# Kernel tuning notes

Measured on AMD Instinct MI355X. Metric: run time of the kernel, lower is better.

Reference implementation:

```python
import jax, jax.numpy as jnp
import numpy as np

B, C, H, W, E = 2, 4, 56, 56, 768
NH = 12
HD = E // NH
WS = 14
MLP_DIM = 3072
EPS = 1e-5


def layernorm(x, w, b):
    mu = jnp.mean(x, axis=-1, keepdims=True)
    var = jnp.mean((x - mu) ** 2, axis=-1, keepdims=True)
    return (x - mu) * jax.lax.rsqrt(var + EPS) * w + b


def setup_inputs() -> dict:
    key = jax.random.key(0)
    ks = jax.random.split(key, 12)
    s = 0.02
    return {
        "x": jax.random.normal(ks[0], (B, C, H, W, E), dtype=jnp.float32),
        "norm1_w": jnp.ones((E,), jnp.float32),
        "norm1_b": jnp.zeros((E,), jnp.float32),
        "qkv_w": jax.random.normal(ks[1], (E, 3 * E), jnp.float32) * s,
        "qkv_b": jnp.zeros((3 * E,), jnp.float32),
        "proj_w": jax.random.normal(ks[2], (E, E), jnp.float32) * s,
        "proj_b": jnp.zeros((E,), jnp.float32),
        "rel_pos_h": jax.random.normal(ks[3], (2 * WS - 1, HD), jnp.float32) * s,
        "rel_pos_w": jax.random.normal(ks[4], (2 * WS - 1, HD), jnp.float32) * s,
        "norm2_w": jnp.ones((E,), jnp.float32),
        "norm2_b": jnp.zeros((E,), jnp.float32),
        "mlp_w1": jax.random.normal(ks[5], (E, MLP_DIM), jnp.float32) * s,
        "mlp_b1": jnp.zeros((MLP_DIM,), jnp.float32),
        "mlp_w2": jax.random.normal(ks[6], (MLP_DIM, E), jnp.float32) * s,
        "mlp_b2": jnp.zeros((E,), jnp.float32),
    }


def reference(x, norm1_w, norm1_b, qkv_w, qkv_b, proj_w, proj_b,
              rel_pos_h, rel_pos_w, norm2_w, norm2_b,
              mlp_w1, mlp_b1, mlp_w2, mlp_b2):
    b, c, h, w, e = x.shape
    scale = HD ** -0.5
    shortcut = x

    y = x.reshape(b * c, h, w, e)
    y = layernorm(y, norm1_w, norm1_b)

    pad_h = (-h) % WS
    pad_w = (-w) % WS
    if pad_h or pad_w:
        y = jnp.pad(y, ((0, 0), (0, pad_h), (0, pad_w), (0, 0)))
    hp, wp = h + pad_h, w + pad_w
    y = y.reshape(b * c, hp // WS, WS, wp // WS, WS, e)
    y = y.transpose(0, 1, 3, 2, 4, 5).reshape(-1, WS, WS, e)  # [Bw, WS, WS, E]
    bw = y.shape[0]
    n = WS * WS

    # qkv projection
    qkv = y.reshape(bw, n, e) @ qkv_w + qkv_b
    qkv = qkv.reshape(bw, n, 3, NH, HD).transpose(2, 0, 3, 1, 4).reshape(3, bw * NH, n, HD)
    q, k, v = qkv[0], qkv[1], qkv[2]

    attn = (q * scale) @ jnp.swapaxes(k, -2, -1)  # [bw*NH, n, n]

    # decomposed relative position bias (q_size == k_size == WS, no interpolation)
    idx = jnp.arange(WS)[:, None] - jnp.arange(WS)[None, :] + (WS - 1)  # [WS, WS]
    Rh = rel_pos_h[idx]  # [WS, WS, HD]
    Rw = rel_pos_w[idx]
    r_q = q.reshape(-1, WS, WS, HD)
    rel_h = jnp.einsum('bhwc,hkc->bhwk', r_q, Rh)
    rel_w = jnp.einsum('bhwc,wkc->bhwk', r_q, Rw)
    attn = (attn.reshape(-1, WS, WS, WS, WS)
            + rel_h[..., :, None]
            + rel_w[:, :, :, None, :]).reshape(-1, n, n)

    attn = jax.nn.softmax(attn, axis=-1)
    out = attn @ v  # [bw*NH, n, HD]
    out = out.reshape(bw, NH, WS, WS, HD).transpose(0, 2, 3, 1, 4).reshape(bw, WS, WS, e)
    out = out @ proj_w + proj_b

    # window unpartition
    out = out.reshape(b * c, hp // WS, wp // WS, WS, WS, e)
    out = out.transpose(0, 1, 3, 2, 4, 5).reshape(b * c, hp, wp, e)
    out = out[:, :h, :w, :].reshape(b, c, h, w, e)

    x1 = shortcut + out
    z = layernorm(x1, norm2_w, norm2_b)
    z = jax.nn.gelu(z @ mlp_w1 + mlp_b1, approximate=False)
    z = z @ mlp_w2 + mlp_b2
    return x1 + z
```

## Files before the change

kernel.cpp:

```cpp
#include <hip/hip_runtime.h>
#include <math.h>

typedef unsigned short u16;
typedef __bf16 bf16x8 __attribute__((ext_vector_type(8)));
typedef float   f32x4 __attribute__((ext_vector_type(4)));
typedef u16     u16x4 __attribute__((ext_vector_type(4)));

#define TOK 25088
#define EMB 768
#define NWH 1536
#define NTOKW 196
#define PROW 224
#define PPAD 232
#define GROUP_M 4

#define OFF_VT 38535168ull
#define OFF_W0 127565824ull
#define OFF_W1 131104768ull
#define OFF_W2 132284416ull
#define OFF_W3 137003008ull
#define OFF_H  38535168ull

__device__ __forceinline__ u16 f2bf(float f) {
  __bf16 h = (__bf16)f;
  return __builtin_bit_cast(u16, h);
}

__device__ __forceinline__ float bf2f(u16 u) {
  return __builtin_bit_cast(float, (unsigned)u << 16);
}

__device__ __forceinline__ void cp16(void* lds, const void* gsrc) {
  __builtin_amdgcn_global_load_lds((const __attribute__((address_space(1))) void*)gsrc,
                                   (__attribute__((address_space(3))) void*)lds,
                                   16, 0, 0);
}

__device__ __forceinline__ f32x4 mfma16(bf16x8 a, bf16x8 b, f32x4 c) {
  return __builtin_amdgcn_mfma_f32_16x16x32_bf16(a, b, c, 0, 0, 0);
}

__global__ __launch_bounds__(256)
void transpose_w(const float* __restrict__ src, u16* __restrict__ dst, int R, int C) {
  __shared__ float tile[32][33];
  const int tx = threadIdx.x & 31;
  const int ty = threadIdx.x >> 5;
  const int c0 = blockIdx.x * 32;
  const int r0 = blockIdx.y * 32;
  #pragma unroll
  for (int i = ty; i < 32; i += 8)
    tile[i][tx] = src[(size_t)(r0 + i) * C + c0 + tx];
  __syncthreads();
  #pragma unroll
  for (int i = ty; i < 32; i += 8)
    dst[(size_t)(c0 + i) * R + r0 + tx] = f2bf(tile[tx][i]);
}

template<bool WIN>
__global__ __launch_bounds__(256)
void ln_kernel(const float* __restrict__ x, const float* __restrict__ g,
               const float* __restrict__ b, u16* __restrict__ y) {
  const int wave = threadIdx.x >> 6;
  const int lane = threadIdx.x & 63;
  const int row = blockIdx.x * 4 + wave;
  const float* xr = x + (size_t)row * EMB;
  float4 v[3];
  float s = 0.f, ss = 0.f;
  #pragma unroll
  for (int j = 0; j < 3; j++) {
    v[j] = *(const float4*)&xr[lane * 4 + j * 256];
    s  += v[j].x + v[j].y + v[j].z + v[j].w;
    ss += v[j].x*v[j].x + v[j].y*v[j].y + v[j].z*v[j].z + v[j].w*v[j].w;
  }
  #pragma unroll
  for (int off = 1; off < 64; off <<= 1) {
    s  += __shfl_xor(s, off);
    ss += __shfl_xor(ss, off);
  }
  const float mu = s * (1.0f / 768.0f);
  const float var = ss * (1.0f / 768.0f) - mu * mu;
  const float rs = rsqrtf(var + 1e-5f);
  size_t drow;
  if (WIN) {
    const int bc = row / 3136;
    const int rem = row - bc * 3136;
    const int h = rem / 56;
    const int w = rem - h * 56;
    const int window = bc * 16 + (h / 14) * 4 + (w / 14);
    const int token = (h % 14) * 14 + (w % 14);
    drow = (size_t)window * NTOKW + token;
  } else {
    drow = (size_t)row;
  }
  u16* yr = y + drow * EMB;
  #pragma unroll
  for (int j = 0; j < 3; j++) {
    const int e = lane * 4 + j * 256;
    const float4 gv = *(const float4*)&g[e];
    const float4 bv = *(const float4*)&b[e];
    u16x4 o;
    o[0] = f2bf((v[j].x - mu) * rs * gv.x + bv.x);
    o[1] = f2bf((v[j].y - mu) * rs * gv.y + bv.y);
    o[2] = f2bf((v[j].z - mu) * rs * gv.z + bv.z);
    o[3] = f2bf((v[j].w - mu) * rs * gv.w + bv.w);
    *(u16x4*)&yr[e] = o;
  }
}

#define EPI_QKV  0
#define EPI_PROJ 1
#define EPI_MLP1 2
#define EPI_MLP2 3

template<int EPI>
__global__ __launch_bounds__(512, 2)
void gemm256(const u16* __restrict__ A, const u16* __restrict__ Bt,
             int K, int moff, int nbm, int nbn,
             const float* __restrict__ bias,
             const float* __restrict__ aux,
             u16* __restrict__ o0, u16* __restrict__ o1, u16* __restrict__ o2,
             float* of) {
  __shared__ __align__(16) u16 lds[2][2][256 * 64];
  const int t = threadIdx.x;
  const int wave = t >> 6;
  const int lane = t & 63;
  const int quad = lane >> 4;
  const int l16 = lane & 15;
  const int wm = wave >> 2;
  const int wn = wave & 3;

  const int in_group = GROUP_M * nbn;
  const int gid = blockIdx.x / in_group;
  const int rem0 = blockIdx.x - gid * in_group;
  const int gm = min(GROUP_M, nbm - gid * GROUP_M);
  const int bm = gid * GROUP_M + rem0 % gm;
  const int bn = rem0 / gm;
  const int m0 = bm * 256;
  const int n0 = bn * 256;

  const int sr0 = t >> 3;
  const int sc0 = ((t ^ (t >> 3)) & 7) * 8;
  const int c1_ = t + 512;
  const int sr1 = c1_ >> 3;
  const int sc1 = ((c1_ ^ (c1_ >> 3)) & 7) * 8;
  const u16* Ag0 = A + (size_t)(m0 + sr0) * K + sc0;
  const u16* Ag1 = A + (size_t)(m0 + sr1) * K + sc1;
  const u16* Bg0 = Bt + (size_t)(n0 + sr0) * K + sc0;
  const u16* Bg1 = Bt + (size_t)(n0 + sr1) * K + sc1;
  const size_t hstep = (size_t)128 * K;

  const int cK0 = ((quad    ) ^ (l16 & 7)) * 8;
  const int cK1 = ((4 + quad) ^ (l16 & 7)) * 8;

  f32x4 acc[8][4];
  const f32x4 zero4 = {0.f, 0.f, 0.f, 0.f};
  #pragma unroll
  for (int i = 0; i < 8; i++)
    #pragma unroll
    for (int j = 0; j < 4; j++) acc[i][j] = zero4;
  bf16x8 bfr[4][2];

#define STG(bb, mat, half, G0, G1, kk) do {                                          \
    cp16(&lds[bb][mat][(half) * 8192 + wave * 512],        (G0) + (half) * hstep + (kk)); \
    cp16(&lds[bb][mat][(half) * 8192 + 4096 + wave * 512], (G1) + (half) * hstep + (kk)); \
  } while (0)

#define LOADB(bb) do {                                                               \
    _Pragma("unroll")                                                                \
    for (int nf = 0; nf < 4; nf++) {                                                 \
      bfr[nf][0] = *(const bf16x8*)&lds[bb][1][(wn * 64 + nf * 16 + l16) * 64 + cK0];\
      bfr[nf][1] = *(const bf16x8*)&lds[bb][1][(wn * 64 + nf * 16 + l16) * 64 + cK1];\
    }                                                                                \
  } while (0)

#define PHASE(bb, slab, PRE, POST) do {                                              \
    const int ar_ = (wm * 128 + (slab) * 32 + l16) * 64;                             \
    bf16x8 a00 = *(const bf16x8*)&lds[bb][0][ar_ + cK0];                             \
    bf16x8 a01 = *(const bf16x8*)&lds[bb][0][ar_ + cK1];                             \
    bf16x8 a10 = *(const bf16x8*)&lds[bb][0][ar_ + 1024 + cK0];                      \
    bf16x8 a11 = *(const bf16x8*)&lds[bb][0][ar_ + 1024 + cK1];                      \
    PRE;                                                                             \
    __builtin_amdgcn_s_barrier();                                                    \
    asm volatile("s_waitcnt lgkmcnt(0)" ::: "memory");                               \
    __builtin_amdgcn_sched_barrier(0);                                               \
    __builtin_amdgcn_s_setprio(1);                                                   \
    _Pragma("unroll")                                                                \
    for (int nf = 0; nf < 4; nf++) {                                                 \
      acc[(slab) * 2    ][nf] = mfma16(a00, bfr[nf][0], acc[(slab) * 2    ][nf]);    \
      acc[(slab) * 2    ][nf] = mfma16(a01, bfr[nf][1], acc[(slab) * 2    ][nf]);    \
      acc[(slab) * 2 + 1][nf] = mfma16(a10, bfr[nf][0], acc[(slab) * 2 + 1][nf]);    \
      acc[(slab) * 2 + 1][nf] = mfma16(a11, bfr[nf][1], acc[(slab) * 2 + 1][nf]);    \
    }                                                                                \
    __builtin_amdgcn_s_setprio(0);                                                   \
    POST;                                                                            \
    __builtin_amdgcn_s_barrier();                                                    \
  } while (0)

  STG(0, 1, 0, Bg0, Bg1, 0);  STG(0, 1, 1, Bg0, Bg1, 0);
  STG(0, 0, 0, Ag0, Ag1, 0);  STG(0, 0, 1, Ag0, Ag1, 0);
  STG(1, 1, 0, Bg0, Bg1, 64); STG(1, 1, 1, Bg0, Bg1, 64);
  asm volatile("s_waitcnt vmcnt(4)" ::: "memory");
  __builtin_amdgcn_s_barrier();

  const int T = K >> 7;
  for (int it = 0; it < T; ++it) {
    const bool nlast = (it < T - 1);
    const int kA1 = (2 * it + 1) << 6;
    const int kT2 = (2 * it + 2) << 6;
    const int kT3 = (2 * it + 3) << 6;

    LOADB(0);
    PHASE(0, 0, STG(1, 0, 0, Ag0, Ag1, kA1), );
    PHASE(0, 1, STG(1, 0, 1, Ag0, Ag1, kA1), );
    PHASE(0, 2, if (nlast) STG(0, 1, 0, Bg0, Bg1, kT2), );
    PHASE(0, 3, if (nlast) STG(0, 1, 1, Bg0, Bg1, kT2),
          if (nlast) { asm volatile("s_waitcnt vmcnt(4)" ::: "memory"); }
          else       { asm volatile("s_waitcnt vmcnt(0)" ::: "memory"); }
          __builtin_amdgcn_sched_barrier(0); );
    LOADB(1);
    PHASE(1, 0, if (nlast) STG(0, 0, 0, Ag0, Ag1, kT2), );
    PHASE(1, 1, if (nlast) STG(0, 0, 1, Ag0, Ag1, kT2), );
    PHASE(1, 2, if (nlast) STG(1, 1, 0, Bg0, Bg1, kT3), );
    PHASE(1, 3, if (nlast) STG(1, 1, 1, Bg0, Bg1, kT3),
          asm volatile("s_waitcnt vmcnt(4)" ::: "memory");
          __builtin_amdgcn_sched_barrier(0); );
  }
#undef STG
#undef LOADB
#undef PHASE

  #pragma unroll
  for (int mf = 0; mf < 8; mf++) {
    const int mb = m0 + wm * 128 + mf * 16 + quad * 4;
    #pragma unroll
    for (int nf = 0; nf < 4; nf++) {
      const int n = n0 + wn * 64 + nf * 16 + l16;
      const float bn_ = bias[n];
      if (EPI == EPI_QKV) {
        const int j3 = n / 768;
        const int rem = n - j3 * 768;
        const int head = rem >> 6;
        const int d = rem & 63;
        if (j3 == 2) {
          const int window = mb / 196;
          const int token = mb - window * 196;
          const int wh = window * 12 + head;
          u16x4 pv;
          #pragma unroll
          for (int r = 0; r < 4; r++) pv[r] = f2bf(acc[mf][nf][r] + bn_);
          *(u16x4*)&o2[((size_t)wh * 64 + d) * PROW + token] = pv;
        } else {
          u16* dst = (j3 == 0) ? o0 : o1;
          #pragma unroll
          for (int r = 0; r < 4; r++) {
            const int m = mb + r;
            const int window = m / 196;
            const int token = m - window * 196;
            const int wh = window * 12 + head;
            dst[((size_t)wh * NTOKW + token) * 64 + d] = f2bf(acc[mf][nf][r] + bn_);
          }
        }
      } else if (EPI == EPI_PROJ) {
        #pragma unroll
        for (int r = 0; r < 4; r++) {
          const int m = mb + r;
          const int window = m / 196;
          const int token = m - window * 196;
          const int bc = window >> 4;
          const int wi = window & 15;
          const int th = token / 14;
          const int tw = token - th * 14;
          const int h = (wi >> 2) * 14 + th;
          const int w = (wi & 3) * 14 + tw;
          const size_t flat = (((size_t)bc * 56 + h) * 56 + w) * 768 + n;
          of[flat] = acc[mf][nf][r] + bn_ + aux[flat];
        }
      } else if (EPI == EPI_MLP1) {
        #pragma unroll
        for (int r = 0; r < 4; r++) {
          const int m = mb + r;
          float v = acc[mf][nf][r] + bn_;
          v = 0.5f * v * (1.0f + erff(v * 0.70710678118654752f));
          o0[(size_t)m * 3072 + n] = f2bf(v);
        }
      } else {
        #pragma unroll
        for (int r = 0; r < 4; r++) {
          const int m = mb + r + moff;
          const size_t idx = (size_t)m * 768 + n;
          of[idx] = acc[mf][nf][r] + bn_ + aux[idx];
        }
      }
    }
  }
}

__global__ __launch_bounds__(256, 2)
void attn_fused(const u16* __restrict__ q, const u16* __restrict__ k,
                const u16* __restrict__ vT,
                const float* __restrict__ rph, const float* __restrict__ rpw,
                u16* __restrict__ out) {
  __shared__ __align__(16) u16 lsK[208 * 64];
  __shared__ __align__(16) u16 relh[16 * 224];
  __shared__ __align__(16) u16 relw[16 * 224];
  __shared__ __align__(16) u16 lsP[4][16 * PPAD];
  const int t = threadIdx.x;
  const int wave = t >> 6;
  const int lane = t & 63;
  const int quad = lane >> 4;
  const int l16 = lane & 15;
  const int wh = blockIdx.x;
  const u16* qg = q + (size_t)wh * (NTOKW * 64);
  const u16* kg = k + (size_t)wh * (NTOKW * 64);
  const u16* vg = vT + (size_t)wh * 64 * PROW;
  const int window = wh / 12;
  const int head = wh - window * 12;

  #pragma unroll
  for (int i = 0; i < 6; i++) {
    const int chunk = i * 256 + t;
    const int goff = ((chunk & ~7) | ((chunk ^ (chunk >> 3)) & 7)) * 8;
    cp16(lsK + (i * 256 + wave * 64) * 8, kg + goff);
  }
  if (t < 32) {
    const int chunk = 1536 + t;
    const int goff = ((chunk & ~7) | ((chunk ^ (chunk >> 3)) & 7)) * 8;
    cp16(lsK + 1536 * 8, kg + goff);
  }

  const f32x4 zero4 = {0.f, 0.f, 0.f, 0.f};
  for (int tile = wave; tile < 14; tile += 4) {
    f32x4 ah = zero4, aw = zero4;
    const int ridx = min(max(tile - l16 + 13, 0), 26);
    #pragma unroll
    for (int ks = 0; ks < 2; ks++) {
      const int ko = ks * 32 + quad * 8;
      bf16x8 aq_h = *(const bf16x8*)&qg[(tile * 14 + l16) * 64 + ko];
      bf16x8 aq_w = *(const bf16x8*)&qg[(tile + 14 * l16) * 64 + ko];
      bf16x8 bh, bw;
      const float* ph = rph + ridx * 64 + ko;
      const float* pw = rpw + ridx * 64 + ko;
      #pragma unroll
      for (int e = 0; e < 8; e++) { bh[e] = (__bf16)ph[e]; bw[e] = (__bf16)pw[e]; }
      ah = mfma16(aq_h, bh, ah);
      aw = mfma16(aq_w, bw, aw);
    }
    #pragma unroll
    for (int r = 0; r < 4; r++) {
      const int m = quad * 4 + r;
      if (m < 14) {
        relh[l16 * 224 + tile * 14 + m] = f2bf(ah[r]);
        relw[l16 * 224 + tile + 14 * m] = f2bf(aw[r]);
      }
    }
  }
  __syncthreads();

  const float scale = 0.125f;
  const int sw = l16 & 7;
  u16* myP = &lsP[wave][0];
  for (int s = wave; s < 13; s += 4) {
    bf16x8 aq[2];
    #pragma unroll
    for (int ks = 0; ks < 2; ks++)
      aq[ks] = *(const bf16x8*)&qg[(s * 16 + l16) * 64 + ks * 32 + quad * 8];
    f32x4 acc[13];
    #pragma unroll
    for (int jt = 0; jt < 13; jt++) {
      f32x4 a = zero4;
      a = mfma16(aq[0], *(const bf16x8*)&lsK[(jt * 16 + l16) * 64 + (quad ^ sw) * 8], a);
      a = mfma16(aq[1], *(const bf16x8*)&lsK[(jt * 16 + l16) * 64 + ((quad + 4) ^ sw) * 8], a);
      acc[jt] = a;
    }
    f32x4 mx = {-1e30f, -1e30f, -1e30f, -1e30f};
    #pragma unroll
    for (int jt = 0; jt < 13; jt++) {
      const int col = jt * 16 + l16;
      if (col < 196) {
        const int kh = col / 14;
        const int kw = col - kh * 14;
        const u16x4 rhu = *(const u16x4*)&relh[kh * 224 + s * 16 + quad * 4];
        const u16x4 rwu = *(const u16x4*)&relw[kw * 224 + s * 16 + quad * 4];
        #pragma unroll
        for (int r = 0; r < 4; r++)
          acc[jt][r] = acc[jt][r] * scale + bf2f(rhu[r]) + bf2f(rwu[r]);
      } else {
        acc[jt] = (f32x4){-1e30f, -1e30f, -1e30f, -1e30f};
      }
      #pragma unroll
      for (int r = 0; r < 4; r++) mx[r] = fmaxf(mx[r], acc[jt][r]);
    }
    #pragma unroll
    for (int off = 1; off < 16; off <<= 1)
      #pragma unroll
      for (int r = 0; r < 4; r++) mx[r] = fmaxf(mx[r], __shfl_xor(mx[r], off));
    f32x4 sum = zero4;
    #pragma unroll
    for (int jt = 0; jt < 13; jt++)
      #pragma unroll
      for (int r = 0; r < 4; r++) {
        const float p = exp2f((acc[jt][r] - mx[r]) * 1.4426950408889634f);
        acc[jt][r] = p;
        sum[r] += p;
      }
    #pragma unroll
    for (int off = 1; off < 16; off <<= 1)
      #pragma unroll
      for (int r = 0; r < 4; r++) sum[r] += __shfl_xor(sum[r], off);
    #pragma unroll
    for (int r = 0; r < 4; r++) {
      const float rinv = 1.0f / sum[r];
      const int prow = (quad * 4 + r) * PPAD;
      #pragma unroll
      for (int jt = 0; jt < 13; jt++)
        myP[prow + jt * 16 + l16] = f2bf(acc[jt][r] * rinv);
      myP[prow + 208 + l16] = 0;
    }
    asm volatile("s_waitcnt lgkmcnt(0)" ::: "memory");
    f32x4 acco[4] = {zero4, zero4, zero4, zero4};
    #pragma unroll
    for (int ks = 0; ks < 7; ks++) {
      bf16x8 ap = *(const bf16x8*)&myP[l16 * PPAD + ks * 32 + quad * 8];
      #pragma unroll
      for (int nt = 0; nt < 4; nt++) {
        bf16x8 bv = *(const bf16x8*)&vg[(nt * 16 + l16) * PROW + ks * 32 + quad * 8];
        acco[nt] = mfma16(ap, bv, acco[nt]);
      }
    }
    #pragma unroll
    for (int nt = 0; nt < 4; nt++)
      #pragma unroll
      for (int r = 0; r < 4; r++) {
        const int i = s * 16 + quad * 4 + r;
        if (i < 196)
          out[((size_t)window * NTOKW + i) * EMB + head * 64 + nt * 16 + l16] =
              f2bf(acco[nt][r]);
      }
  }
}

extern "C" void kernel_launch(void* const* d_in, const int* in_sizes, int n_in,
                              void* d_out, int out_size, void* d_ws, size_t ws_size,
                              hipStream_t stream) {
  const float* x      = (const float*)d_in[0];
  const float* n1w    = (const float*)d_in[1];
  const float* n1b    = (const float*)d_in[2];
  const float* qkv_w  = (const float*)d_in[3];
  const float* qkv_b  = (const float*)d_in[4];
  const float* proj_w = (const float*)d_in[5];
  const float* proj_b = (const float*)d_in[6];
  const float* rph    = (const float*)d_in[7];
  const float* rpw    = (const float*)d_in[8];
  const float* n2w    = (const float*)d_in[9];
  const float* n2b    = (const float*)d_in[10];
  const float* w1     = (const float*)d_in[11];
  const float* b1     = (const float*)d_in[12];
  const float* w2     = (const float*)d_in[13];
  const float* b2     = (const float*)d_in[14];
  float* out = (float*)d_out;

  char* ws = (char*)d_ws;
  u16* bufT   = (u16*)(ws);
  u16* vTb    = (u16*)(ws + OFF_VT);
  u16* hb     = (u16*)(ws + OFF_H);
  u16* wqkvT  = (u16*)(ws + OFF_W0);
  u16* wprojT = (u16*)(ws + OFF_W1);
  u16* w1T    = (u16*)(ws + OFF_W2);
  u16* w2T    = (u16*)(ws + OFF_W3);
  u16* qb = (u16*)d_out;
  u16* kb = qb + (size_t)19267584;

  dim3 blk(256), blkg(512);
  transpose_w<<<dim3(72, 24), blk, 0, stream>>>(qkv_w, wqkvT, 768, 2304);
  transpose_w<<<dim3(24, 24), blk, 0, stream>>>(proj_w, wprojT, 768, 768);
  transpose_w<<<dim3(96, 24), blk, 0, stream>>>(w1, w1T, 768, 3072);
  transpose_w<<<dim3(24, 96), blk, 0, stream>>>(w2, w2T, 3072, 768);

  ln_kernel<true><<<6272, blk, 0, stream>>>(x, n1w, n1b, bufT);

  gemm256<EPI_QKV><<<98 * 9, blkg, 0, stream>>>(
      bufT, wqkvT, 768, 0, 98, 9, qkv_b, nullptr, qb, kb, vTb, nullptr);

  attn_fused<<<NWH, blk, 0, stream>>>(qb, kb, vTb, rph, rpw, bufT);

  gemm256<EPI_PROJ><<<98 * 3, blkg, 0, stream>>>(
      bufT, wprojT, 768, 0, 98, 3, proj_b, x, nullptr, nullptr, nullptr, out);

  ln_kernel<false><<<6272, blk, 0, stream>>>(out, n2w, n2b, bufT);

  for (int c = 0; c < 2; c++) {
    const int row0 = c * 12544;
    gemm256<EPI_MLP1><<<49 * 12, blkg, 0, stream>>>(
        bufT + (size_t)row0 * 768, w1T, 768, 0, 49, 12, b1, nullptr, hb, nullptr, nullptr, nullptr);
    gemm256<EPI_MLP2><<<49 * 3, blkg, 0, stream>>>(
        hb, w2T, 3072, row0, 49, 3, b2, out, nullptr, nullptr, nullptr, out);
  }

  (void)in_sizes; (void)n_in; (void)out_size; (void)ws_size;
}
```

Baseline: 992.9 us.

## Use smaller 128x128 GEMM kernel for narrow proj/MLP2 GEMMs and XCD-aware block mapping

Adds a 128x128-tile, 256-thread GEMM (gemm_bt) and uses it for the projection and MLP2 GEMMs, whose N=768 gave too few 256x256 blocks (294 and 147) to fill the GPU. It also adds a block remapping that assigns contiguous logical tiles to each XCD, so neighbouring tiles share L2, and applies it to both GEMM kernels. The new kernel has no double buffering and synchronises twice per 32-wide K step, so it may lose per-block efficiency compared with the larger pipelined kernel.

```diff
diff --git a/kernel.cpp b/kernel.cpp
--- a/kernel.cpp
+++ b/kernel.cpp
@@ -38,6 +38,19 @@
 
 __device__ __forceinline__ f32x4 mfma16(bf16x8 a, bf16x8 b, f32x4 c) {
   return __builtin_amdgcn_mfma_f32_16x16x32_bf16(a, b, c, 0, 0, 0);
+}
+
+__device__ __forceinline__ void map_block(int b, int nwg, int nbm, int nbn,
+                                          int* bm, int* bn) {
+  const int q = nwg >> 3, r = nwg & 7;
+  const int xcd = b & 7, slot = b >> 3;
+  const int logical = (xcd < r ? xcd * (q + 1) : r * (q + 1) + (xcd - r) * q) + slot;
+  const int in_group = GROUP_M * nbn;
+  const int gid = logical / in_group;
+  const int rem0 = logical - gid * in_group;
+  const int gm = min(GROUP_M, nbm - gid * GROUP_M);
+  *bm = gid * GROUP_M + rem0 % gm;
+  *bn = rem0 / gm;
 }
 
 __global__ __launch_bounds__(256)
@@ -129,12 +142,8 @@
   const int wm = wave >> 2;
   const int wn = wave & 3;
 
-  const int in_group = GROUP_M * nbn;
-  const int gid = blockIdx.x / in_group;
-  const int rem0 = blockIdx.x - gid * in_group;
-  const int gm = min(GROUP_M, nbm - gid * GROUP_M);
-  const int bm = gid * GROUP_M + rem0 % gm;
-  const int bn = rem0 / gm;
+  int bm, bn;
+  map_block(blockIdx.x, gridDim.x, nbm, nbn, &bm, &bn);
   const int m0 = bm * 256;
   const int n0 = bn * 256;
 
@@ -260,7 +269,90 @@
             dst[((size_t)wh * NTOKW + token) * 64 + d] = f2bf(acc[mf][nf][r] + bn_);
           }
         }
-      } else if (EPI == EPI_PROJ) {
+      } else if (EPI == EPI_MLP1) {
+        #pragma unroll
+        for (int r = 0; r < 4; r++) {
+          const int m = mb + r;
+          float v = acc[mf][nf][r] + bn_;
+          v = 0.5f * v * (1.0f + erff(v * 0.70710678118654752f));
+          o0[(size_t)m * 3072 + n] = f2bf(v);
+        }
+      }
+    }
+  }
+}
+
+template<int EPI>
+__global__ __launch_bounds__(256, 3)
+void gemm_bt(const u16* __restrict__ A, const u16* __restrict__ Bt,
+             int K, int moff, int nbm, int nbn,
+             const float* __restrict__ bias,
+             const float* __restrict__ aux,
+             u16* __restrict__ o0,
+             float* of) {
+  __shared__ __align__(16) u16 lsA[4096];
+  __shared__ __align__(16) u16 lsB[4096];
+  const int t = threadIdx.x;
+  const int wave = t >> 6;
+  const int lane = t & 63;
+  const int quad = lane >> 4;
+  const int l16 = lane & 15;
+
+  int bm, bn;
+  map_block(blockIdx.x, gridDim.x, nbm, nbn, &bm, &bn);
+  const int m0 = bm * 128;
+  const int n0 = bn * 128;
+
+  const int wm = (wave >> 1) * 64;
+  const int wn = (wave & 1) * 64;
+
+  const int srow = t >> 2;
+  const int scol = (((t & 3) ^ ((t >> 3) & 3))) * 8;
+  const u16* Ag = A + (size_t)(m0 + srow) * K + scol;
+  const u16* Bg = Bt + (size_t)(n0 + srow) * K + scol;
+  u16* lA0 = lsA + wave * 512;
+  u16* lA1 = lsA + 2048 + wave * 512;
+  u16* lB0 = lsB + wave * 512;
+  u16* lB1 = lsB + 2048 + wave * 512;
+
+  const int kc = (quad ^ ((l16 >> 1) & 3)) * 8;
+
+  f32x4 acc[4][4];
+  const f32x4 zero4 = {0.f, 0.f, 0.f, 0.f};
+  #pragma unroll
+  for (int i = 0; i < 4; i++)
+    #pragma unroll
+    for (int j = 0; j < 4; j++) acc[i][j] = zero4;
+
+  for (int k0 = 0; k0 < K; k0 += 32) {
+    cp16(lA0, Ag + k0);
+    cp16(lA1, Ag + (size_t)64 * K + k0);
+    cp16(lB0, Bg + k0);
+    cp16(lB1, Bg + (size_t)64 * K + k0);
+    __syncthreads();
+    bf16x8 af[4], bfr[4];
+    #pragma unroll
+    for (int i = 0; i < 4; i++)
+      af[i] = *(const bf16x8*)&lsA[(wm + i * 16 + l16) * 32 + kc];
+    #pragma unroll
+    for (int j = 0; j < 4; j++)
+      bfr[j] = *(const bf16x8*)&lsB[(wn + j * 16 + l16) * 32 + kc];
+    #pragma unroll
+    for (int i = 0; i < 4; i++)
+      #pragma unroll
+      for (int j = 0; j < 4; j++)
+        acc[i][j] = mfma16(af[i], bfr[j], acc[i][j]);
+    __syncthreads();
+  }
+
+  #pragma unroll
+  for (int i = 0; i < 4; i++) {
+    const int mb = m0 + wm + i * 16 + quad * 4;
+    #pragma unroll
+    for (int j = 0; j < 4; j++) {
+      const int n = n0 + wn + j * 16 + l16;
+      const float bn_ = bias[n];
+      if (EPI == EPI_PROJ) {
         #pragma unroll
         for (int r = 0; r < 4; r++) {
           const int m = mb + r;
@@ -273,22 +365,14 @@
           const int h = (wi >> 2) * 14 + th;
           const int w = (wi & 3) * 14 + tw;
           const size_t flat = (((size_t)bc * 56 + h) * 56 + w) * 768 + n;
-          of[flat] = acc[mf][nf][r] + bn_ + aux[flat];
-        }
-      } else if (EPI == EPI_MLP1) {
-        #pragma unroll
-        for (int r = 0; r < 4; r++) {
-          const int m = mb + r;
-          float v = acc[mf][nf][r] + bn_;
-          v = 0.5f * v * (1.0f + erff(v * 0.70710678118654752f));
-          o0[(size_t)m * 3072 + n] = f2bf(v);
+          of[flat] = acc[i][j][r] + bn_ + aux[flat];
         }
       } else {
         #pragma unroll
         for (int r = 0; r < 4; r++) {
           const int m = mb + r + moff;
           const size_t idx = (size_t)m * 768 + n;
-          of[idx] = acc[mf][nf][r] + bn_ + aux[idx];
+          of[idx] = acc[i][j][r] + bn_ + aux[idx];
         }
       }
     }
@@ -483,8 +567,8 @@
 
   attn_fused<<<NWH, blk, 0, stream>>>(qb, kb, vTb, rph, rpw, bufT);
 
-  gemm256<EPI_PROJ><<<98 * 3, blkg, 0, stream>>>(
-      bufT, wprojT, 768, 0, 98, 3, proj_b, x, nullptr, nullptr, nullptr, out);
+  gemm_bt<EPI_PROJ><<<196 * 6, blk, 0, stream>>>(
+      bufT, wprojT, 768, 0, 196, 6, proj_b, x, nullptr, out);
 
   ln_kernel<false><<<6272, blk, 0, stream>>>(out, n2w, n2b, bufT);
 
@@ -492,8 +576,8 @@
     const int row0 = c * 12544;
     gemm256<EPI_MLP1><<<49 * 12, blkg, 0, stream>>>(
         bufT + (size_t)row0 * 768, w1T, 768, 0, 49, 12, b1, nullptr, hb, nullptr, nullptr, nullptr);
-    gemm256<EPI_MLP2><<<49 * 3, blkg, 0, stream>>>(
-        hb, w2T, 3072, row0, 49, 3, b2, out, nullptr, nullptr, nullptr, out);
+    gemm_bt<EPI_MLP2><<<98 * 6, blk, 0, stream>>>(
+        hb, w2T, 3072, row0, 98, 6, b2, out, nullptr, out);
   }
 
   (void)in_sizes; (void)n_in; (void)out_size; (void)ws_size;
```

New measurement: 955.5 us. 1.04x faster.
